# Kernel optimization log

Measured on AMD Instinct MI355X. Metric: run time of the kernel, lower is better.

The kernel has to match this reference:

```python
import jax, jax.numpy as jnp
import numpy as np
import math

H = 12   # num_attention_heads
DH = 64  # attention_head_size
HID = H * DH  # 768


def setup_inputs() -> dict:
    key = jax.random.key(0)
    ks = jax.random.split(key, 16)
    B, S = 2, 128
    inp = {
        'hidden_states': jax.random.normal(ks[0], (B, S, HID), jnp.float32),
        'attention_mask': jnp.zeros((B, 1, 1, S), jnp.float32),
        'inference_path': jax.random.normal(ks[1], (B, S, S, HID), jnp.float32),
        'span_mask': jax.random.uniform(ks[2], (B, 1, S, S), jnp.float32),
    }
    sc = 1.0 / math.sqrt(HID)
    # weights stored as [in, out]; y = x @ W + b
    inp['Wq'] = jax.random.normal(ks[3], (HID, HID), jnp.float32) * sc
    inp['bq'] = jnp.zeros((HID,), jnp.float32)
    inp['Wk'] = jax.random.normal(ks[4], (HID, HID), jnp.float32) * sc
    inp['bk'] = jnp.zeros((HID,), jnp.float32)
    inp['Wv'] = jax.random.normal(ks[5], (HID, HID), jnp.float32) * sc
    inp['bv'] = jnp.zeros((HID,), jnp.float32)
    inp['Wpv'] = jax.random.normal(ks[6], (HID, DH), jnp.float32) * sc
    inp['bpv'] = jnp.zeros((DH,), jnp.float32)
    inp['Wip'] = jax.random.normal(ks[7], (HID, 2 * HID), jnp.float32) * sc
    inp['Wmlp'] = jax.random.normal(ks[8], (HID + DH, HID), jnp.float32) * sc
    inp['bmlp'] = jnp.zeros((HID,), jnp.float32)
    return inp


def reference(hidden_states, attention_mask, inference_path, span_mask,
              Wq, bq, Wk, bk, Wv, bv, Wpv, bpv, Wip, Wmlp, bmlp):
    B, S, _ = hidden_states.shape
    # projections
    q = (hidden_states @ Wq + bq).reshape(B, S, H, DH).transpose(0, 2, 1, 3)  # [B,H,S,Dh]
    k = (hidden_states @ Wk + bk).reshape(B, S, H, DH).transpose(0, 2, 1, 3)
    v = (hidden_states @ Wv + bv).reshape(B, S, H, DH).transpose(0, 2, 1, 3)
    # parse value path: [B,1,S,Dh]
    pv = (hidden_states @ Wpv + bpv).reshape(B, S, 1, DH).transpose(0, 2, 1, 3)
    parse_ctx = jnp.matmul(span_mask, pv)              # [B,1,S,Dh]
    parse_ctx = parse_ctx.transpose(0, 2, 1, 3)        # [B,S,1,Dh]
    # relative inference-path bias: raw view (matches torch .view semantics)
    ip = inference_path @ Wip                           # [B,S,S,2*HID]
    ra, rb = jnp.split(ip, 2, axis=-1)                  # each [B,S,S,HID]
    ra = ra.reshape(B, H, S, S, DH)
    rb = rb.reshape(B, H, S, S, DH)
    qe = q[:, :, :, None, :] + ra                       # [B,H,S,S,Dh]
    ke = k[:, :, None, :, :] + rb                       # [B,H,S,S,Dh]
    scores = jnp.einsum('bhqkd,bhqkd->bhqk', qe, ke)
    scores = scores / math.sqrt(DH) + attention_mask
    probs = jax.nn.softmax(scores, axis=-1)             # dropout is identity in eval
    ctx = jnp.matmul(probs, v)                          # [B,H,S,Dh]
    ctx = ctx.transpose(0, 2, 1, 3)                     # [B,S,H,Dh]
    ctx = jnp.concatenate([ctx, parse_ctx], axis=-2)    # [B,S,H+1,Dh]
    ctx = ctx.reshape(B, S, HID + DH)
    return ctx @ Wmlp + bmlp                            # [B,S,HID]
```

## Files before the change

kernel.cpp:

```cpp
#include <hip/hip_runtime.h>
#include <hip/hip_bf16.h>


typedef __attribute__((ext_vector_type(8))) __bf16 bf16x8;
typedef __attribute__((ext_vector_type(16))) float f32x16;
typedef __attribute__((ext_vector_type(4))) float f32x4;
typedef __attribute__((ext_vector_type(4))) unsigned int u32x4;

#define QKV_OFF   0u
#define ARENA_OFF 2424832u
#define SC_OFF    4784128u
#define CTX_OFF   6356992u

__global__ __launch_bounds__(256)
void prep_kernel(const float* __restrict__ Wip, __bf16* __restrict__ arena) {
  const int l = threadIdx.x & 63;
  const int f = blockIdx.x * 4 + (threadIdx.x >> 6);
  const int n32 = f / 48, k16 = f - n32 * 48;
  const float* src = Wip + (size_t)(k16 * 16 + (l >> 5) * 8) * 1536 + n32 * 32 + (l & 31);
  union { __bf16 h[8]; uint4 u; } pk;
#pragma unroll
  for (int j = 0; j < 8; j++) pk.h[j] = (__bf16)src[(size_t)j * 1536];
  ((uint4*)arena)[(size_t)f * 64 + l] = pk.u;
}

__global__ __launch_bounds__(64)
void proj_kernel(const float* __restrict__ hs,
                 const float* __restrict__ Wq, const float* __restrict__ bq,
                 const float* __restrict__ Wk, const float* __restrict__ bk,
                 const float* __restrict__ Wv, const float* __restrict__ bv,
                 const float* __restrict__ Wpv, const float* __restrict__ bpv,
                 float* __restrict__ qkv) {
  const int n0 = blockIdx.x * 32;
  const int m0 = blockIdx.y * 32;
  const float* W; const float* bias; int noff, ldw;
  if (n0 < 768)       { W = Wq;  bias = bq;  noff = n0;        ldw = 768; }
  else if (n0 < 1536) { W = Wk;  bias = bk;  noff = n0 - 768;  ldw = 768; }
  else if (n0 < 2304) { W = Wv;  bias = bv;  noff = n0 - 1536; ldw = 768; }
  else                { W = Wpv; bias = bpv; noff = n0 - 2304; ldw = 64;  }
  const int l = threadIdx.x;
  const int rsel = l & 31, ksel = l >> 5;
  f32x16 acc;
#pragma unroll
  for (int z = 0; z < 16; z++) acc[z] = 0.f;

#pragma unroll 4
  for (int k16 = 0; k16 < 48; k16++) {
    const float* ap = hs + (size_t)(m0 + rsel) * 768 + k16 * 16 + ksel * 8;
    float4 a0 = *(const float4*)ap;
    float4 a1 = *(const float4*)(ap + 4);
    union { __bf16 h[8]; bf16x8 v; } pa;
    pa.h[0] = (__bf16)a0.x; pa.h[1] = (__bf16)a0.y; pa.h[2] = (__bf16)a0.z; pa.h[3] = (__bf16)a0.w;
    pa.h[4] = (__bf16)a1.x; pa.h[5] = (__bf16)a1.y; pa.h[6] = (__bf16)a1.z; pa.h[7] = (__bf16)a1.w;
    const float* bp = W + (size_t)(k16 * 16 + ksel * 8) * ldw + noff + rsel;
    union { __bf16 h[8]; bf16x8 v; } pb;
#pragma unroll
    for (int j = 0; j < 8; j++) pb.h[j] = (__bf16)bp[(size_t)j * ldw];
    acc = __builtin_amdgcn_mfma_f32_32x32x16_bf16(pa.v, pb.v, acc, 0, 0, 0);
  }
#pragma unroll
  for (int reg = 0; reg < 16; reg++) {
    int row = (reg & 3) + ((reg >> 2) << 3) + (ksel << 2);
    qkv[(size_t)(m0 + row) * 2368 + n0 + rsel] = acc[reg] + bias[noff + rsel];
  }
}

extern __shared__ char smem_raw[];

__global__ __launch_bounds__(512, 2)
void score_kernel(const float* __restrict__ infp,
                  const __bf16* __restrict__ arena,
                  const float* __restrict__ qkv,
                  float* __restrict__ scores) {
  char* Abase = smem_raw;
  float* lds_sc = (float*)(smem_raw + 99840);
  const int tid = threadIdx.x;
  const int lane = tid & 63;
  const int ml = lane & 31;
  const int kh = lane >> 5;
  const int wv = tid >> 6;
  const int wc = wv & 3;
  const int wd = wv >> 2;
  const int blk = blockIdx.x;
  const int b = blk >> 8;
  const int r0 = (blk & 255) << 6;

  for (int z = tid; z < 768; z += 512) lds_sc[z] = 0.f;

  u32x4 srsrc;
  srsrc[0] = (unsigned)(unsigned long long)arena;
  srsrc[1] = (unsigned)(((unsigned long long)arena) >> 32);
  srsrc[2] = 2359296u;
  srsrc[3] = 0x00020000u;
  const unsigned rbo = 1179648u;
  unsigned voff = (unsigned)((2 * wc + wd) * 49152 + lane * 16);
  int kpn = 0;

  u32x4 B0[8], B1[8], B2[8];
  bf16x8 Af[8];
  f32x16 acc_ra[2], acc_rb[2];

  auto issueB = [&](u32x4* bank) {
    asm volatile("buffer_load_dwordx4 %0, %1, %2, 0 offen offset:0"
                 : "=&v"(bank[0]) : "v"(voff), "s"(srsrc));
    asm volatile("buffer_load_dwordx4 %0, %1, %2, 0 offen offset:1024"
                 : "=&v"(bank[2]) : "v"(voff), "s"(srsrc));
    asm volatile("buffer_load_dwordx4 %0, %1, %2, 0 offen offset:2048"
                 : "=&v"(bank[4]) : "v"(voff), "s"(srsrc));
    asm volatile("buffer_load_dwordx4 %0, %1, %2, 0 offen offset:3072"
                 : "=&v"(bank[6]) : "v"(voff), "s"(srsrc));
    asm volatile("buffer_load_dwordx4 %0, %1, %2, %3 offen offset:0"
                 : "=&v"(bank[1]) : "v"(voff), "s"(srsrc), "s"(rbo));
    asm volatile("buffer_load_dwordx4 %0, %1, %2, %3 offen offset:1024"
                 : "=&v"(bank[3]) : "v"(voff), "s"(srsrc), "s"(rbo));
    asm volatile("buffer_load_dwordx4 %0, %1, %2, %3 offen offset:2048"
                 : "=&v"(bank[5]) : "v"(voff), "s"(srsrc), "s"(rbo));
    asm volatile("buffer_load_dwordx4 %0, %1, %2, %3 offen offset:3072"
                 : "=&v"(bank[7]) : "v"(voff), "s"(srsrc), "s"(rbo));
    if (kpn == 11) { voff += 348160u; kpn = 0; } else { voff += 4096u; kpn++; }
  };

  issueB(B0);
  issueB(B1);
  issueB(B2);

  {
    const f32x4* A4 = (const f32x4*)(infp + (size_t)(b * 16384 + r0) * 768);
#pragma unroll
    for (int p = 0; p < 12; p++) {
      int idx = p * 512 + tid;
      int m = (int)(((unsigned)idx * 10923u) >> 20);
      int g = idx - m * 96;
      f32x4 v0 = __builtin_nontemporal_load(A4 + m * 192 + g * 2);
      f32x4 v1 = __builtin_nontemporal_load(A4 + m * 192 + g * 2 + 1);
      union { __bf16 h[8]; uint4 u; } pk;
      pk.h[0] = (__bf16)v0[0]; pk.h[1] = (__bf16)v0[1];
      pk.h[2] = (__bf16)v0[2]; pk.h[3] = (__bf16)v0[3];
      pk.h[4] = (__bf16)v1[0]; pk.h[5] = (__bf16)v1[1];
      pk.h[6] = (__bf16)v1[2]; pk.h[7] = (__bf16)v1[3];
      int F = (m >> 5) * 48 + (g >> 1);
      int slot = (m & 31) + ((g & 1) << 5);
      *(uint4*)(Abase + ((F * 65 + slot) << 4)) = pk.u;
    }
  }
  __syncthreads();

  const size_t lane_off = (size_t)(lane << 4);
  auto loadA = [&](int kcc) {
    const char* ab = Abase + lane_off + kcc * 4160;
#pragma unroll
    for (int mt = 0; mt < 2; mt++)
#pragma unroll
      for (int ks = 0; ks < 4; ks++)
        Af[mt * 4 + ks] = *(const bf16x8*)(ab + mt * 49920 + ks * 1040);
  };
  auto mfma_step = [&](const u32x4* Bb) {
#pragma unroll
    for (int ks = 0; ks < 4; ks++) {
      bf16x8 bra = __builtin_bit_cast(bf16x8, Bb[ks * 2]);
      bf16x8 brb = __builtin_bit_cast(bf16x8, Bb[ks * 2 + 1]);
#pragma unroll
      for (int mt = 0; mt < 2; mt++) {
        acc_ra[mt] = __builtin_amdgcn_mfma_f32_32x32x16_bf16(Af[mt * 4 + ks], bra, acc_ra[mt], 0, 0, 0);
        acc_rb[mt] = __builtin_amdgcn_mfma_f32_32x32x16_bf16(Af[mt * 4 + ks], brb, acc_rb[mt], 0, 0, 0);
      }
    }
  };
  auto epilogue = [&](int c) {
    int d = wd * 32 + ml;
#pragma unroll
    for (int mt = 0; mt < 2; mt++) {
      float qv[16], kv[16];
#pragma unroll
      for (int reg = 0; reg < 16; reg++) {
        int row = mt * 32 + (reg & 3) + ((reg >> 2) << 3) + (kh << 2);
        int t = 12 * (r0 + row) + c;
        int hh = t >> 14;
        int ii = (t >> 7) & 127;
        int jj = t & 127;
        qv[reg] = qkv[(size_t)((b << 7) + ii) * 2368 + (hh << 6) + d];
        kv[reg] = qkv[(size_t)((b << 7) + jj) * 2368 + 768 + (hh << 6) + d];
      }
#pragma unroll
      for (int reg = 0; reg < 16; reg++) {
        int row = mt * 32 + (reg & 3) + ((reg >> 2) << 3) + (kh << 2);
        float p = (qv[reg] + acc_ra[mt][reg]) * (kv[reg] + acc_rb[mt][reg]);
        p += __shfl_xor(p, 16);
        p += __shfl_xor(p, 8);
        p += __shfl_xor(p, 4);
        p += __shfl_xor(p, 2);
        p += __shfl_xor(p, 1);
        if (ml == 0) atomicAdd(&lds_sc[row * 12 + c], p);
      }
    }
#pragma unroll
    for (int mt = 0; mt < 2; mt++)
#pragma unroll
      for (int z = 0; z < 16; z++) { acc_ra[mt][z] = 0.f; acc_rb[mt][z] = 0.f; }
  };

#pragma unroll
  for (int mt = 0; mt < 2; mt++)
#pragma unroll
    for (int z = 0; z < 16; z++) { acc_ra[mt][z] = 0.f; acc_rb[mt][z] = 0.f; }

#define WAIT16 do { asm volatile("s_waitcnt vmcnt(16)" ::: "memory"); __builtin_amdgcn_sched_barrier(0); } while (0)
#define WAIT8  do { asm volatile("s_waitcnt vmcnt(8)"  ::: "memory"); __builtin_amdgcn_sched_barrier(0); } while (0)
#define WAIT0  do { asm volatile("s_waitcnt vmcnt(0)"  ::: "memory"); __builtin_amdgcn_sched_barrier(0); } while (0)

  int kc = 0, c = wc;
#pragma unroll 1
  for (int it = 0; it < 11; it++) {
    {
      loadA(kc); WAIT16; mfma_step(B0); issueB(B0);
      if (kc == 11) { epilogue(c); kc = 0; c += 4; } else kc++;
    }
    {
      loadA(kc); WAIT16; mfma_step(B1); issueB(B1);
      if (kc == 11) { epilogue(c); kc = 0; c += 4; } else kc++;
    }
    {
      loadA(kc); WAIT16; mfma_step(B2); issueB(B2);
      if (kc == 11) { epilogue(c); kc = 0; c += 4; } else kc++;
    }
  }
  loadA(kc); WAIT16; mfma_step(B0); kc++;
  loadA(kc); WAIT8;  mfma_step(B1); kc++;
  loadA(kc); WAIT0;  mfma_step(B2); epilogue(c);

#undef WAIT16
#undef WAIT8
#undef WAIT0

  __syncthreads();
  for (int z = tid; z < 768; z += 512) {
    int row = z / 12;
    int ccc = z - row * 12;
    int t = 12 * (r0 + row) + ccc;
    int hh = t >> 14;
    int ii = (t >> 7) & 127;
    int jj = t & 127;
    scores[(size_t)((b * 12 + hh) * 128 + ii) * 128 + jj] = lds_sc[z];
  }
}

__global__ __launch_bounds__(256)
void attn_kernel(const float* __restrict__ scores, const float* __restrict__ qkv,
                 const float* __restrict__ mask, const float* __restrict__ span,
                 float* __restrict__ ctx) {
  const int i = blockIdx.x;
  const int b = blockIdx.y;
  const int tid = threadIdx.x;
  const int l = tid & 63;
  const int wvi = tid >> 6;
  __shared__ float w[13][132];
  for (int r = wvi; r < 13; r += 4) {
    if (r < 12) {
      const float* sp = scores + (size_t)((b * 12 + r) * 128 + i) * 128;
      float s0 = sp[l] * 0.125f + mask[b * 128 + l];
      float s1 = sp[l + 64] * 0.125f + mask[b * 128 + l + 64];
      float mx = fmaxf(s0, s1);
#pragma unroll
      for (int o = 32; o; o >>= 1) mx = fmaxf(mx, __shfl_xor(mx, o));
      float e0 = __expf(s0 - mx), e1 = __expf(s1 - mx);
      float sm = e0 + e1;
#pragma unroll
      for (int o = 32; o; o >>= 1) sm += __shfl_xor(sm, o);
      float inv = 1.f / sm;
      w[r][l] = e0 * inv;
      w[r][l + 64] = e1 * inv;
    } else {
      const float* sp = span + (size_t)(b * 128 + i) * 128;
      w[12][l] = sp[l];
      w[12][l + 64] = sp[l + 64];
    }
  }
  __syncthreads();
  for (int o = tid; o < 832; o += 256) {
    int h = o >> 6, d = o & 63;
    const float* vp = qkv + (size_t)(b * 128) * 2368 + (h < 12 ? 1536 + h * 64 : 2304) + d;
    float acc = 0.f;
#pragma unroll 8
    for (int j = 0; j < 128; j++) acc += w[h][j] * vp[(size_t)j * 2368];
    ctx[(size_t)(b * 128 + i) * 832 + o] = acc;
  }
}

__global__ __launch_bounds__(64)
void out_kernel(const float* __restrict__ ctxb, const float* __restrict__ Wmlp,
                const float* __restrict__ bmlp, float* __restrict__ out) {
  const int n0 = blockIdx.x * 32;
  const int m0 = blockIdx.y * 32;
  const int l = threadIdx.x;
  const int rsel = l & 31, ksel = l >> 5;
  f32x16 acc;
#pragma unroll
  for (int z = 0; z < 16; z++) acc[z] = 0.f;

#pragma unroll 4
  for (int k16 = 0; k16 < 52; k16++) {
    const float* ap = ctxb + (size_t)(m0 + rsel) * 832 + k16 * 16 + ksel * 8;
    float4 a0 = *(const float4*)ap;
    float4 a1 = *(const float4*)(ap + 4);
    union { __bf16 h[8]; bf16x8 v; } pa;
    pa.h[0] = (__bf16)a0.x; pa.h[1] = (__bf16)a0.y; pa.h[2] = (__bf16)a0.z; pa.h[3] = (__bf16)a0.w;
    pa.h[4] = (__bf16)a1.x; pa.h[5] = (__bf16)a1.y; pa.h[6] = (__bf16)a1.z; pa.h[7] = (__bf16)a1.w;
    const float* bp = Wmlp + (size_t)(k16 * 16 + ksel * 8) * 768 + n0 + rsel;
    union { __bf16 h[8]; bf16x8 v; } pb;
#pragma unroll
    for (int j = 0; j < 8; j++) pb.h[j] = (__bf16)bp[(size_t)j * 768];
    acc = __builtin_amdgcn_mfma_f32_32x32x16_bf16(pa.v, pb.v, acc, 0, 0, 0);
  }
#pragma unroll
  for (int reg = 0; reg < 16; reg++) {
    int row = (reg & 3) + ((reg >> 2) << 3) + (ksel << 2);
    out[(size_t)(m0 + row) * 768 + n0 + rsel] = acc[reg] + bmlp[n0 + rsel];
  }
}

extern "C" void kernel_launch(void* const* d_in, const int* in_sizes, int n_in,
                              void* d_out, int out_size, void* d_ws, size_t ws_size,
                              hipStream_t stream) {
  const float* hs   = (const float*)d_in[0];
  const float* mask = (const float*)d_in[1];
  const float* infp = (const float*)d_in[2];
  const float* span = (const float*)d_in[3];
  const float* Wq   = (const float*)d_in[4];
  const float* bq   = (const float*)d_in[5];
  const float* Wk   = (const float*)d_in[6];
  const float* bk   = (const float*)d_in[7];
  const float* Wv   = (const float*)d_in[8];
  const float* bv   = (const float*)d_in[9];
  const float* Wpv  = (const float*)d_in[10];
  const float* bpv  = (const float*)d_in[11];
  const float* Wip  = (const float*)d_in[12];
  const float* Wmlp = (const float*)d_in[13];
  const float* bmlp = (const float*)d_in[14];
  float* out = (float*)d_out;

  char* ws = (char*)d_ws;
  float*  qkv    = (float*)(ws + QKV_OFF);
  __bf16* arena  = (__bf16*)(ws + ARENA_OFF);
  float*  scores = (float*)(ws + SC_OFF);
  float*  ctx    = (float*)(ws + CTX_OFF);

  prep_kernel<<<dim3(576), 256, 0, stream>>>(Wip, arena);
  proj_kernel<<<dim3(74, 8), 64, 0, stream>>>(hs, Wq, bq, Wk, bk, Wv, bv, Wpv, bpv, qkv);
  score_kernel<<<dim3(512), 512, 102912, stream>>>(infp, arena, qkv, scores);
  attn_kernel<<<dim3(128, 2), 256, 0, stream>>>(scores, qkv, mask, span, ctx);
  out_kernel<<<dim3(24, 8), 64, 0, stream>>>(ctx, Wmlp, bmlp, out);
}
```

Before: 408.8 us.

## Reuse weight fragments across four M tiles and reorder score kernel B prefetch

The projection and output GEMM kernels now compute four 32-row M tiles per block. Each converted weight fragment feeds four MFMAs, so weight global loads and fp32-to-bf16 conversions drop fourfold, but the grid shrinks fourfold and fewer waves are in flight. In the score kernel, the initial B-buffer prefetch now starts after the A tile is staged into LDS instead of before it. The launch bound also changes from 2 to 1 blocks per CU, which gives the compiler more registers at a possible occupancy cost.

```diff
diff --git a/kernel.cpp b/kernel.cpp
--- a/kernel.cpp
+++ b/kernel.cpp
@@ -32,7 +32,7 @@
                  const float* __restrict__ Wpv, const float* __restrict__ bpv,
                  float* __restrict__ qkv) {
   const int n0 = blockIdx.x * 32;
-  const int m0 = blockIdx.y * 32;
+  const int msup = blockIdx.y * 128;
   const float* W; const float* bias; int noff, ldw;
   if (n0 < 768)       { W = Wq;  bias = bq;  noff = n0;        ldw = 768; }
   else if (n0 < 1536) { W = Wk;  bias = bk;  noff = n0 - 768;  ldw = 768; }
@@ -40,34 +40,41 @@
   else                { W = Wpv; bias = bpv; noff = n0 - 2304; ldw = 64;  }
   const int l = threadIdx.x;
   const int rsel = l & 31, ksel = l >> 5;
-  f32x16 acc;
-#pragma unroll
-  for (int z = 0; z < 16; z++) acc[z] = 0.f;
-
-#pragma unroll 4
+  f32x16 acc[4];
+#pragma unroll
+  for (int mi = 0; mi < 4; mi++)
+#pragma unroll
+    for (int z = 0; z < 16; z++) acc[mi][z] = 0.f;
+
+#pragma unroll 2
   for (int k16 = 0; k16 < 48; k16++) {
-    const float* ap = hs + (size_t)(m0 + rsel) * 768 + k16 * 16 + ksel * 8;
-    float4 a0 = *(const float4*)ap;
-    float4 a1 = *(const float4*)(ap + 4);
-    union { __bf16 h[8]; bf16x8 v; } pa;
-    pa.h[0] = (__bf16)a0.x; pa.h[1] = (__bf16)a0.y; pa.h[2] = (__bf16)a0.z; pa.h[3] = (__bf16)a0.w;
-    pa.h[4] = (__bf16)a1.x; pa.h[5] = (__bf16)a1.y; pa.h[6] = (__bf16)a1.z; pa.h[7] = (__bf16)a1.w;
     const float* bp = W + (size_t)(k16 * 16 + ksel * 8) * ldw + noff + rsel;
     union { __bf16 h[8]; bf16x8 v; } pb;
 #pragma unroll
     for (int j = 0; j < 8; j++) pb.h[j] = (__bf16)bp[(size_t)j * ldw];
-    acc = __builtin_amdgcn_mfma_f32_32x32x16_bf16(pa.v, pb.v, acc, 0, 0, 0);
-  }
-#pragma unroll
-  for (int reg = 0; reg < 16; reg++) {
-    int row = (reg & 3) + ((reg >> 2) << 3) + (ksel << 2);
-    qkv[(size_t)(m0 + row) * 2368 + n0 + rsel] = acc[reg] + bias[noff + rsel];
-  }
+#pragma unroll
+    for (int mi = 0; mi < 4; mi++) {
+      const float* ap = hs + (size_t)(msup + mi * 32 + rsel) * 768 + k16 * 16 + ksel * 8;
+      float4 a0 = *(const float4*)ap;
+      float4 a1 = *(const float4*)(ap + 4);
+      union { __bf16 h[8]; bf16x8 v; } pa;
+      pa.h[0] = (__bf16)a0.x; pa.h[1] = (__bf16)a0.y; pa.h[2] = (__bf16)a0.z; pa.h[3] = (__bf16)a0.w;
+      pa.h[4] = (__bf16)a1.x; pa.h[5] = (__bf16)a1.y; pa.h[6] = (__bf16)a1.z; pa.h[7] = (__bf16)a1.w;
+      acc[mi] = __builtin_amdgcn_mfma_f32_32x32x16_bf16(pa.v, pb.v, acc[mi], 0, 0, 0);
+    }
+  }
+#pragma unroll
+  for (int mi = 0; mi < 4; mi++)
+#pragma unroll
+    for (int reg = 0; reg < 16; reg++) {
+      int row = msup + mi * 32 + (reg & 3) + ((reg >> 2) << 3) + (ksel << 2);
+      qkv[(size_t)row * 2368 + n0 + rsel] = acc[mi][reg] + bias[noff + rsel];
+    }
 }
 
 extern __shared__ char smem_raw[];
 
-__global__ __launch_bounds__(512, 2)
+__global__ __launch_bounds__(512, 1)
 void score_kernel(const float* __restrict__ infp,
                   const __bf16* __restrict__ arena,
                   const float* __restrict__ qkv,
@@ -120,10 +127,6 @@
     if (kpn == 11) { voff += 348160u; kpn = 0; } else { voff += 4096u; kpn++; }
   };
 
-  issueB(B0);
-  issueB(B1);
-  issueB(B2);
-
   {
     const f32x4* A4 = (const f32x4*)(infp + (size_t)(b * 16384 + r0) * 768);
 #pragma unroll
@@ -144,6 +147,10 @@
     }
   }
   __syncthreads();
+
+  issueB(B0);
+  issueB(B1);
+  issueB(B2);
 
   const size_t lane_off = (size_t)(lane << 4);
   auto loadA = [&](int kcc) {
@@ -290,32 +297,39 @@
 void out_kernel(const float* __restrict__ ctxb, const float* __restrict__ Wmlp,
                 const float* __restrict__ bmlp, float* __restrict__ out) {
   const int n0 = blockIdx.x * 32;
-  const int m0 = blockIdx.y * 32;
+  const int msup = blockIdx.y * 128;
   const int l = threadIdx.x;
   const int rsel = l & 31, ksel = l >> 5;
-  f32x16 acc;
-#pragma unroll
-  for (int z = 0; z < 16; z++) acc[z] = 0.f;
-
-#pragma unroll 4
+  f32x16 acc[4];
+#pragma unroll
+  for (int mi = 0; mi < 4; mi++)
+#pragma unroll
+    for (int z = 0; z < 16; z++) acc[mi][z] = 0.f;
+
+#pragma unroll 2
   for (int k16 = 0; k16 < 52; k16++) {
-    const float* ap = ctxb + (size_t)(m0 + rsel) * 832 + k16 * 16 + ksel * 8;
-    float4 a0 = *(const float4*)ap;
-    float4 a1 = *(const float4*)(ap + 4);
-    union { __bf16 h[8]; bf16x8 v; } pa;
-    pa.h[0] = (__bf16)a0.x; pa.h[1] = (__bf16)a0.y; pa.h[2] = (__bf16)a0.z; pa.h[3] = (__bf16)a0.w;
-    pa.h[4] = (__bf16)a1.x; pa.h[5] = (__bf16)a1.y; pa.h[6] = (__bf16)a1.z; pa.h[7] = (__bf16)a1.w;
     const float* bp = Wmlp + (size_t)(k16 * 16 + ksel * 8) * 768 + n0 + rsel;
     union { __bf16 h[8]; bf16x8 v; } pb;
 #pragma unroll
     for (int j = 0; j < 8; j++) pb.h[j] = (__bf16)bp[(size_t)j * 768];
-    acc = __builtin_amdgcn_mfma_f32_32x32x16_bf16(pa.v, pb.v, acc, 0, 0, 0);
-  }
-#pragma unroll
-  for (int reg = 0; reg < 16; reg++) {
-    int row = (reg & 3) + ((reg >> 2) << 3) + (ksel << 2);
-    out[(size_t)(m0 + row) * 768 + n0 + rsel] = acc[reg] + bmlp[n0 + rsel];
-  }
+#pragma unroll
+    for (int mi = 0; mi < 4; mi++) {
+      const float* ap = ctxb + (size_t)(msup + mi * 32 + rsel) * 832 + k16 * 16 + ksel * 8;
+      float4 a0 = *(const float4*)ap;
+      float4 a1 = *(const float4*)(ap + 4);
+      union { __bf16 h[8]; bf16x8 v; } pa;
+      pa.h[0] = (__bf16)a0.x; pa.h[1] = (__bf16)a0.y; pa.h[2] = (__bf16)a0.z; pa.h[3] = (__bf16)a0.w;
+      pa.h[4] = (__bf16)a1.x; pa.h[5] = (__bf16)a1.y; pa.h[6] = (__bf16)a1.z; pa.h[7] = (__bf16)a1.w;
+      acc[mi] = __builtin_amdgcn_mfma_f32_32x32x16_bf16(pa.v, pb.v, acc[mi], 0, 0, 0);
+    }
+  }
+#pragma unroll
+  for (int mi = 0; mi < 4; mi++)
+#pragma unroll
+    for (int reg = 0; reg < 16; reg++) {
+      int row = msup + mi * 32 + (reg & 3) + ((reg >> 2) << 3) + (ksel << 2);
+      out[(size_t)row * 768 + n0 + rsel] = acc[mi][reg] + bmlp[n0 + rsel];
+    }
 }
 
 extern "C" void kernel_launch(void* const* d_in, const int* in_sizes, int n_in,
@@ -345,8 +359,8 @@
   float*  ctx    = (float*)(ws + CTX_OFF);
 
   prep_kernel<<<dim3(576), 256, 0, stream>>>(Wip, arena);
-  proj_kernel<<<dim3(74, 8), 64, 0, stream>>>(hs, Wq, bq, Wk, bk, Wv, bv, Wpv, bpv, qkv);
+  proj_kernel<<<dim3(74, 2), 64, 0, stream>>>(hs, Wq, bq, Wk, bk, Wv, bv, Wpv, bpv, qkv);
   score_kernel<<<dim3(512), 512, 102912, stream>>>(infp, arena, qkv, scores);
   attn_kernel<<<dim3(128, 2), 256, 0, stream>>>(scores, qkv, mask, span, ctx);
-  out_kernel<<<dim3(24, 8), 64, 0, stream>>>(ctx, Wmlp, bmlp, out);
-}
+  out_kernel<<<dim3(24, 2), 64, 0, stream>>>(ctx, Wmlp, bmlp, out);
+}
```

Measured after the change: 392.3 us. 1.04x faster.
